# Kernel optimization log

Hardware: AMD Instinct MI355X
Metric: run time of the kernel (lower is better)

The kernel has to match this reference:

```python
import jax, jax.numpy as jnp
import numpy as np
import math

E = 1024      # embed_dim
H = 16        # num_heads
D = 32        # head_dim = E // H // 2
DEPTH = 12
LAMBDA_INIT = 0.8 - 0.6 * math.exp(-0.3 * DEPTH)
B, T = 4, 1024
EPS = 1e-5


def setup_inputs() -> dict:
    key = jax.random.key(0)
    ks = jax.random.split(key, 10)
    s = 0.02  # realistic init scale for weight matrices
    return {
        "x": jax.random.normal(ks[0], (B, T, E), jnp.float32),
        "Wq": jax.random.normal(ks[1], (E, E), jnp.float32) * s,
        "Wk": jax.random.normal(ks[2], (E, E), jnp.float32) * s,
        "Wv": jax.random.normal(ks[3], (E, E), jnp.float32) * s,
        "Wo": jax.random.normal(ks[4], (E, E), jnp.float32) * s,
        "lambda_q1": jax.random.normal(ks[5], (D,), jnp.float32) * 0.1,
        "lambda_k1": jax.random.normal(ks[6], (D,), jnp.float32) * 0.1,
        "lambda_q2": jax.random.normal(ks[7], (D,), jnp.float32) * 0.1,
        "lambda_k2": jax.random.normal(ks[8], (D,), jnp.float32) * 0.1,
        "g": jnp.ones((2 * D,), jnp.float32),  # subln affine weight
    }


def reference(x, Wq, Wk, Wv, Wo, lambda_q1, lambda_k1, lambda_q2, lambda_k2, g):
    b, t, _ = x.shape
    scaling = D ** -0.5
    # projections (torch Linear: x @ W.T), split into 2H half-width q/k heads
    q = (x @ Wq.T).reshape(b, t, 2 * H, D).transpose(0, 2, 1, 3) * scaling  # [b,2H,t,D]
    k = (x @ Wk.T).reshape(b, t, 2 * H, D).transpose(0, 2, 1, 3)            # [b,2H,t,D]
    v = (x @ Wv.T).reshape(b, t, H, 2 * D).transpose(0, 2, 1, 3)            # [b,H,t,2D]
    # dual score maps, fp32 softmax
    aw = jnp.einsum('bhqd,bhkd->bhqk', q, k)               # [b,2H,t,t]
    aw = jnp.nan_to_num(aw)
    aw = jax.nn.softmax(aw.astype(jnp.float32), axis=-1).astype(q.dtype)
    # scalar lambda
    lam1 = jnp.exp(jnp.sum(lambda_q1 * lambda_k1))
    lam2 = jnp.exp(jnp.sum(lambda_q2 * lambda_k2))
    lam = lam1 - lam2 + LAMBDA_INIT
    # differential subtract of the paired softmax maps
    aw = aw.reshape(b, H, 2, t, t)
    aw = aw[:, :, 0] - lam * aw[:, :, 1]                   # [b,H,t,t]
    attn = jnp.einsum('bhqk,bhkd->bhqd', aw, v)            # [b,H,t,2D]
    # per-head RMSNorm over 2D channel dim (affine)
    attn = attn * jax.lax.rsqrt(jnp.mean(attn * attn, axis=-1, keepdims=True) + EPS) * g
    attn = attn * (1.0 - LAMBDA_INIT)
    attn = attn.transpose(0, 2, 1, 3).reshape(b, t, H * 2 * D)  # [b,t,E]
    return attn @ Wo.T
```

## Files before the change

kernel.cpp:

```cpp
#include <hip/hip_runtime.h>
#include <math.h>

#define E_   1024
#define H_   16
#define B_   4
#define T_   1024
#define LAMBDA_INIT 0.783605766532f
#define SCALE_QL2E 0.25503486f

typedef short s16x8 __attribute__((ext_vector_type(8)));
typedef float f32x4 __attribute__((ext_vector_type(4)));

#define SWZ(c, r) ((((c) ^ ((r) & 7)) * 8))

__device__ inline ushort f2bf(float x) {
    unsigned u = __builtin_bit_cast(unsigned, x);
    u += 0x7fffu + ((u >> 16) & 1u);
    return (ushort)(u >> 16);
}

__device__ inline uint f2bf2(float lo, float hi) {
#if __has_builtin(__builtin_amdgcn_cvt_pk_bf16_f32)
    typedef __bf16 bf16x2_t __attribute__((ext_vector_type(2)));
    bf16x2_t r = __builtin_amdgcn_cvt_pk_bf16_f32(lo, hi);
    return __builtin_bit_cast(uint, r);
#else
    uint ul = __builtin_bit_cast(uint, lo);
    uint uh = __builtin_bit_cast(uint, hi);
    ul += 0x7fffu + ((ul >> 16) & 1u);
    uh += 0x7fffu + ((uh >> 16) & 1u);
    return __builtin_amdgcn_perm(uh, ul, 0x07060302u);
#endif
}

__device__ inline float exp2fast(float x) {
#if __has_builtin(__builtin_amdgcn_exp2f)
    return __builtin_amdgcn_exp2f(x);
#else
    return exp2f(x);
#endif
}

__device__ inline void gl_lds16(const ushort* g, ushort* l) {
    __builtin_amdgcn_global_load_lds((const __attribute__((address_space(1))) void*)g,
                                     (__attribute__((address_space(3))) void*)l,
                                     16, 0, 0);
}

__global__ __launch_bounds__(256) void prep(
    const float* __restrict__ x,  const float* __restrict__ Wq,
    const float* __restrict__ Wk, const float* __restrict__ Wv,
    const float* __restrict__ Wo,
    const float* __restrict__ lq1, const float* __restrict__ lk1,
    const float* __restrict__ lq2, const float* __restrict__ lk2,
    ushort* __restrict__ xb, ushort* __restrict__ Wqb, ushort* __restrict__ Wkb,
    ushort* __restrict__ Wvb, ushort* __restrict__ Wob, float* __restrict__ lamp)
{
    const int blk = blockIdx.x;
    const int tid = threadIdx.x;
    if (blk >= 4096) {
        if (tid < 64) {
            float p1 = 0.f, p2 = 0.f;
            if (tid < 32) { p1 = lq1[tid] * lk1[tid]; p2 = lq2[tid] * lk2[tid]; }
            #pragma unroll
            for (int off = 32; off; off >>= 1) {
                p1 += __shfl_xor(p1, off);
                p2 += __shfl_xor(p2, off);
            }
            if (tid == 0) lamp[0] = expf(p1) - expf(p2) + LAMBDA_INIT;
        }
        return;
    }
    const float* in;
    ushort* out;
    int base;
    if (blk < 2048) { in = x; out = xb; base = blk; }
    else {
        int t = blk - 2048, w = t >> 9;
        base = t & 511;
        in  = w == 0 ? Wq  : (w == 1 ? Wk  : (w == 2 ? Wv  : Wo));
        out = w == 0 ? Wqb : (w == 1 ? Wkb : (w == 2 ? Wvb : Wob));
    }
    int i = (base * 256 + tid) * 8;
    float4 a = *(const float4*)&in[i];
    float4 b = *(const float4*)&in[i + 4];
    union { ushort u[8]; uint4 v; } o;
    o.u[0] = f2bf(a.x); o.u[1] = f2bf(a.y); o.u[2] = f2bf(a.z); o.u[3] = f2bf(a.w);
    o.u[4] = f2bf(b.x); o.u[5] = f2bf(b.y); o.u[6] = f2bf(b.z); o.u[7] = f2bf(b.w);
    *(uint4*)&out[i] = o.v;
}

__global__ __launch_bounds__(256) void gemm_qkv(
    const ushort* __restrict__ Xb, const ushort* __restrict__ Wqb,
    const ushort* __restrict__ Wkb, const ushort* __restrict__ Wvb,
    ushort* __restrict__ QK, ushort* __restrict__ Vt)
{
    __shared__ ushort As[128 * 32];
    __shared__ ushort Ws[128 * 32];
    const int tid = threadIdx.x;
    const int wave = tid >> 6, lane = tid & 63;
    const int l15 = lane & 15, quad = lane >> 4;
    const int bm = blockIdx.y * 128;
    const int bng = blockIdx.x * 128;
    const int region = bng >> 10;
    const ushort* W = region == 0 ? Wqb : (region == 1 ? Wkb : Wvb);
    const float scale = region == 0 ? SCALE_QL2E : 1.0f;
    const int wn = bng & 1023;
    const int lrow = lane >> 2;
    const int lcol = (lane & 3) * 8;

    f32x4 acc[4][4] = {};
    const int wr = wave >> 1, wc = wave & 1;

    for (int k0 = 0; k0 < 1024; k0 += 32) {
        #pragma unroll
        for (int p = 0; p < 2; ++p) {
            int i = wave + 4 * p;
            gl_lds16(&Xb[(size_t)(bm + i * 16 + lrow) * 1024 + k0 + lcol], &As[i * 512]);
            gl_lds16(&W [(size_t)(wn + i * 16 + lrow) * 1024 + k0 + lcol], &Ws[i * 512]);
        }
        __syncthreads();
        s16x8 a[4], b[4];
        #pragma unroll
        for (int i = 0; i < 4; ++i)
            a[i] = *(const s16x8*)&As[(wr * 64 + i * 16 + l15) * 32 + quad * 8];
        #pragma unroll
        for (int j = 0; j < 4; ++j)
            b[j] = *(const s16x8*)&Ws[(wc * 64 + j * 16 + l15) * 32 + quad * 8];
        if (region < 2) {
            #pragma unroll
            for (int i = 0; i < 4; ++i)
                #pragma unroll
                for (int j = 0; j < 4; ++j)
                    acc[i][j] = __builtin_amdgcn_mfma_f32_16x16x32_bf16(b[j], a[i], acc[i][j], 0, 0, 0);
        } else {
            #pragma unroll
            for (int i = 0; i < 4; ++i)
                #pragma unroll
                for (int j = 0; j < 4; ++j)
                    acc[i][j] = __builtin_amdgcn_mfma_f32_16x16x32_bf16(a[i], b[j], acc[i][j], 0, 0, 0);
        }
        __syncthreads();
    }

    if (region < 2) {
        #pragma unroll
        for (int i = 0; i < 4; ++i) {
            int row = bm + wr * 64 + i * 16 + l15;
            #pragma unroll
            for (int j = 0; j < 4; ++j) {
                int col = region * 1024 + wn + wc * 64 + j * 16 + quad * 4;
                ushort4 o;
                o.x = f2bf(acc[i][j][0] * scale); o.y = f2bf(acc[i][j][1] * scale);
                o.z = f2bf(acc[i][j][2] * scale); o.w = f2bf(acc[i][j][3] * scale);
                *(ushort4*)&QK[(size_t)row * 2048 + col] = o;
            }
        }
    } else {
        const int bb = bm >> 10;
        const int t0 = (bm & 1023) + wr * 64 + quad * 4;
        #pragma unroll
        for (int i = 0; i < 4; ++i)
            #pragma unroll
            for (int j = 0; j < 4; ++j) {
                int e = wn + wc * 64 + j * 16 + l15;
                ushort4 o;
                o.x = f2bf(acc[i][j][0]); o.y = f2bf(acc[i][j][1]);
                o.z = f2bf(acc[i][j][2]); o.w = f2bf(acc[i][j][3]);
                *(ushort4*)&Vt[((size_t)bb * E_ + e) * T_ + t0 + i * 16] = o;
            }
    }
}

__global__ __launch_bounds__(256) void gemm_out(
    const ushort* __restrict__ Ab, const ushort* __restrict__ Wob,
    float* __restrict__ C)
{
    __shared__ ushort As[64 * 32];
    __shared__ ushort Ws[128 * 32];
    const int tid = threadIdx.x;
    const int wave = tid >> 6, lane = tid & 63;
    const int l15 = lane & 15, quad = lane >> 4;
    const int bm = blockIdx.y * 64;
    const int bn = blockIdx.x * 128;
    const int lrow = lane >> 2;
    const int lcol = (lane & 3) * 8;

    f32x4 acc[2][4] = {};
    const int wr = wave >> 1, wc = wave & 1;

    for (int k0 = 0; k0 < 1024; k0 += 32) {
        gl_lds16(&Ab[(size_t)(bm + wave * 16 + lrow) * 1024 + k0 + lcol], &As[wave * 512]);
        #pragma unroll
        for (int p = 0; p < 2; ++p) {
            int i = wave + 4 * p;
            gl_lds16(&Wob[(size_t)(bn + i * 16 + lrow) * 1024 + k0 + lcol], &Ws[i * 512]);
        }
        __syncthreads();
        s16x8 a[2], b[4];
        #pragma unroll
        for (int i = 0; i < 2; ++i)
            a[i] = *(const s16x8*)&As[(wr * 32 + i * 16 + l15) * 32 + quad * 8];
        #pragma unroll
        for (int j = 0; j < 4; ++j)
            b[j] = *(const s16x8*)&Ws[(wc * 64 + j * 16 + l15) * 32 + quad * 8];
        #pragma unroll
        for (int i = 0; i < 2; ++i)
            #pragma unroll
            for (int j = 0; j < 4; ++j)
                acc[i][j] = __builtin_amdgcn_mfma_f32_16x16x32_bf16(b[j], a[i], acc[i][j], 0, 0, 0);
        __syncthreads();
    }

    #pragma unroll
    for (int i = 0; i < 2; ++i) {
        int row = bm + wr * 32 + i * 16 + l15;
        #pragma unroll
        for (int j = 0; j < 4; ++j) {
            int col = bn + wc * 64 + j * 16 + quad * 4;
            float4 o;
            o.x = acc[i][j][0]; o.y = acc[i][j][1];
            o.z = acc[i][j][2]; o.w = acc[i][j][3];
            *(float4*)&C[(size_t)row * 1024 + col] = o;
        }
    }
}

__global__ __launch_bounds__(256, 4) void diff_attn(
    const ushort* __restrict__ QK, const ushort* __restrict__ Vt,
    const float* __restrict__ g, const float* __restrict__ lamp,
    ushort* __restrict__ O)
{
    __shared__ __align__(16) ushort Ks[2][4096];
    __shared__ __align__(16) ushort Vts[2][4096];
    __shared__ __align__(16) ushort Pt[4][1024];

    const int tid  = threadIdx.x;
    const int lane = tid & 63;
    const int wave = tid >> 6;
    const int l15  = lane & 15;
    const int quad = lane >> 4;

    const int blk = blockIdx.x;
    const int bh = blk & 63;
    const int qt = blk >> 6;
    const int b  = bh >> 4;
    const int h  = bh & 15;
    const int q0 = qt * 64;
    const int hoff = h * 64;
    const size_t rowbase = (size_t)b * T_;

    const ushort* Qg = QK;
    const ushort* Kg = QK + 1024;
    const size_t vtbase = ((size_t)b * E_ + hoff) * T_;

    const int lr  = lane >> 3;
    const int jsw = ((lane & 7) ^ lr) * 8;

    const size_t qrow = (rowbase + q0 + wave * 16 + l15) * 2048 + hoff;
    s16x8 aq0 = *(const s16x8*)&Qg[qrow + quad * 8];
    s16x8 aq1 = *(const s16x8*)&Qg[qrow + 32 + quad * 8];

    const int kaoff0 = l15 * 64 + SWZ(quad,     l15);
    const int kaoff1 = l15 * 64 + SWZ(4 + quad, l15);
    ushort* myPt = &Pt[wave][0];

    const f32x4 zf = {0.f, 0.f, 0.f, 0.f};
    f32x4 o0[4] = {zf, zf, zf, zf};
    f32x4 o1[4] = {zf, zf, zf, zf};
    float lsum0 = 0.f, lsum1 = 0.f;

    #pragma unroll
    for (int p = 0; p < 2; ++p) {
        int r = wave * 16 + p * 8;
        gl_lds16(&Kg[(rowbase + r + lr) * 2048 + hoff + jsw], &Ks[0][r * 64]);
        gl_lds16(&Vt[vtbase + (size_t)(r + lr) * T_ + jsw],   &Vts[0][r * 64]);
    }
    __syncthreads();

    for (int kt = 0; kt < 16; ++kt) {
        const int cur = kt & 1;
        const int nxt = cur ^ 1;
        {
            const int ktn = (kt + 1) & 15;
            #pragma unroll
            for (int p = 0; p < 2; ++p) {
                int r = wave * 16 + p * 8;
                gl_lds16(&Kg[(rowbase + ktn * 64 + r + lr) * 2048 + hoff + jsw],
                         &Ks[nxt][r * 64]);
                gl_lds16(&Vt[vtbase + (size_t)(r + lr) * T_ + ktn * 64 + jsw],
                         &Vts[nxt][r * 64]);
            }
        }

        s16x8 va[4][2];
        #pragma unroll
        for (int jt = 0; jt < 4; ++jt) {
            va[jt][0] = *(const s16x8*)&Vts[cur][jt * 1024 + kaoff0];
            va[jt][1] = *(const s16x8*)&Vts[cur][jt * 1024 + kaoff1];
        }

        {
            f32x4 S[4];
            #pragma unroll
            for (int jk = 0; jk < 4; ++jk) {
                s16x8 ka = *(const s16x8*)&Ks[cur][jk * 1024 + kaoff0];
                S[jk] = __builtin_amdgcn_mfma_f32_16x16x32_bf16(ka, aq0, zf, 0, 0, 0);
            }
            #pragma unroll
            for (int jk = 0; jk < 4; ++jk) {
                float e0 = exp2fast(S[jk][0]), e1 = exp2fast(S[jk][1]);
                float e2 = exp2fast(S[jk][2]), e3 = exp2fast(S[jk][3]);
                lsum0 += (e0 + e1) + (e2 + e3);
                uint2 pk; pk.x = f2bf2(e0, e1); pk.y = f2bf2(e2, e3);
                *(uint2*)&myPt[l15 * 64 + SWZ(2 * jk + (quad >> 1), l15) + (quad & 1) * 4] = pk;
            }
            #pragma unroll
            for (int h2 = 0; h2 < 2; ++h2) {
                s16x8 pf = *(const s16x8*)&myPt[h2 ? kaoff1 : kaoff0];
                #pragma unroll
                for (int jt = 0; jt < 4; ++jt)
                    o0[jt] = __builtin_amdgcn_mfma_f32_16x16x32_bf16(va[jt][h2], pf, o0[jt], 0, 0, 0);
            }
        }
        {
            f32x4 S[4];
            #pragma unroll
            for (int jk = 0; jk < 4; ++jk) {
                s16x8 ka = *(const s16x8*)&Ks[cur][jk * 1024 + kaoff1];
                S[jk] = __builtin_amdgcn_mfma_f32_16x16x32_bf16(ka, aq1, zf, 0, 0, 0);
            }
            #pragma unroll
            for (int jk = 0; jk < 4; ++jk) {
                float e0 = exp2fast(S[jk][0]), e1 = exp2fast(S[jk][1]);
                float e2 = exp2fast(S[jk][2]), e3 = exp2fast(S[jk][3]);
                lsum1 += (e0 + e1) + (e2 + e3);
                uint2 pk; pk.x = f2bf2(e0, e1); pk.y = f2bf2(e2, e3);
                *(uint2*)&myPt[l15 * 64 + SWZ(2 * jk + (quad >> 1), l15) + (quad & 1) * 4] = pk;
            }
            #pragma unroll
            for (int h2 = 0; h2 < 2; ++h2) {
                s16x8 pf = *(const s16x8*)&myPt[h2 ? kaoff1 : kaoff0];
                #pragma unroll
                for (int jt = 0; jt < 4; ++jt)
                    o1[jt] = __builtin_amdgcn_mfma_f32_16x16x32_bf16(va[jt][h2], pf, o1[jt], 0, 0, 0);
            }
        }
        __syncthreads();
    }

    lsum0 += __shfl_xor(lsum0, 16); lsum0 += __shfl_xor(lsum0, 32);
    lsum1 += __shfl_xor(lsum1, 16); lsum1 += __shfl_xor(lsum1, 32);

    const float lam = lamp[0];
    const float fin = 1.f - LAMBDA_INIT;
    float i0 = 1.f / lsum0;
    float i1 = lam / lsum1;
    float val[4][4];
    float ssq = 0.f;
    #pragma unroll
    for (int jt = 0; jt < 4; ++jt)
        #pragma unroll
        for (int r = 0; r < 4; ++r) {
            float v = o0[jt][r] * i0 - o1[jt][r] * i1;
            val[jt][r] = v;
            ssq += v * v;
        }
    ssq += __shfl_xor(ssq, 16);
    ssq += __shfl_xor(ssq, 32);
    float sc = rsqrtf(ssq * (1.f / 64.f) + 1e-5f) * fin;
    size_t rowoff = (rowbase + q0 + wave * 16 + l15) * 1024 + hoff;
    #pragma unroll
    for (int jt = 0; jt < 4; ++jt) {
        float4 gv = *(const float4*)&g[jt * 16 + quad * 4];
        uint p01 = f2bf2(val[jt][0] * sc * gv.x, val[jt][1] * sc * gv.y);
        uint p23 = f2bf2(val[jt][2] * sc * gv.z, val[jt][3] * sc * gv.w);
        *(uint*)&O[rowoff + jt * 16 + quad * 4 + 0] = p01;
        *(uint*)&O[rowoff + jt * 16 + quad * 4 + 2] = p23;
    }
}

extern "C" void kernel_launch(void* const* d_in, const int* in_sizes, int n_in,
                              void* d_out, int out_size, void* d_ws, size_t ws_size,
                              hipStream_t stream)
{
    const float* x   = (const float*)d_in[0];
    const float* Wq  = (const float*)d_in[1];
    const float* Wk  = (const float*)d_in[2];
    const float* Wv  = (const float*)d_in[3];
    const float* Wo  = (const float*)d_in[4];
    const float* lq1 = (const float*)d_in[5];
    const float* lk1 = (const float*)d_in[6];
    const float* lq2 = (const float*)d_in[7];
    const float* lk2 = (const float*)d_in[8];
    const float* g   = (const float*)d_in[9];
    float* out = (float*)d_out;

    const int M = B_ * T_;
    const size_t ME = (size_t)M * E_;
    const size_t EE = (size_t)E_ * E_;
    ushort* xb  = (ushort*)d_ws;
    ushort* Wqb = xb  + ME;
    ushort* Wkb = Wqb + EE;
    ushort* Wvb = Wkb + EE;
    ushort* Wob = Wvb + EE;
    ushort* QK  = Wob + EE;
    ushort* Vtb = QK + (size_t)M * 2048;
    float*  lamp = (float*)(Vtb + ME);
    ushort* Ab  = xb;

    prep<<<4097, 256, 0, stream>>>(x, Wq, Wk, Wv, Wo, lq1, lk1, lq2, lk2,
                                   xb, Wqb, Wkb, Wvb, Wob, lamp);
    gemm_qkv<<<dim3(24, 32), 256, 0, stream>>>(xb, Wqb, Wkb, Wvb, QK, Vtb);
    diff_attn<<<B_ * H_ * (T_ / 64), 256, 0, stream>>>(QK, Vtb, g, lamp, Ab);
    gemm_out<<<dim3(8, 64), 256, 0, stream>>>(Ab, Wob, out);
}
```

Before: 203.9 us.

## Double-buffer LDS tiles and XOR-swizzle columns in projection GEMMs

Both the QKV and output projection GEMMs now prefetch the next K-tile into a second LDS buffer while computing on the current one. This aims to hide global-to-LDS latency behind MFMA work. The LDS column index is also XOR-swizzled by row to reduce bank conflicts on fragment reads. LDS use doubles, which may reduce occupancy.

```diff
diff --git a/kernel.cpp b/kernel.cpp
--- a/kernel.cpp
+++ b/kernel.cpp
@@ -95,8 +95,8 @@
     const ushort* __restrict__ Wkb, const ushort* __restrict__ Wvb,
     ushort* __restrict__ QK, ushort* __restrict__ Vt)
 {
-    __shared__ ushort As[128 * 32];
-    __shared__ ushort Ws[128 * 32];
+    __shared__ ushort As[2][128 * 32];
+    __shared__ ushort Ws[2][128 * 32];
     const int tid = threadIdx.x;
     const int wave = tid >> 6, lane = tid & 63;
     const int l15 = lane & 15, quad = lane >> 4;
@@ -107,26 +107,38 @@
     const float scale = region == 0 ? SCALE_QL2E : 1.0f;
     const int wn = bng & 1023;
     const int lrow = lane >> 2;
-    const int lcol = (lane & 3) * 8;
+    const int lcol = ((lane & 3) ^ (lrow & 3)) * 8;
+    const int sw8 = (quad ^ (l15 & 3)) * 8;
 
     f32x4 acc[4][4] = {};
     const int wr = wave >> 1, wc = wave & 1;
 
-    for (int k0 = 0; k0 < 1024; k0 += 32) {
-        #pragma unroll
-        for (int p = 0; p < 2; ++p) {
-            int i = wave + 4 * p;
-            gl_lds16(&Xb[(size_t)(bm + i * 16 + lrow) * 1024 + k0 + lcol], &As[i * 512]);
-            gl_lds16(&W [(size_t)(wn + i * 16 + lrow) * 1024 + k0 + lcol], &Ws[i * 512]);
-        }
-        __syncthreads();
+    #pragma unroll
+    for (int p = 0; p < 2; ++p) {
+        int i = wave + 4 * p;
+        gl_lds16(&Xb[(size_t)(bm + i * 16 + lrow) * 1024 + lcol], &As[0][i * 512]);
+        gl_lds16(&W [(size_t)(wn + i * 16 + lrow) * 1024 + lcol], &Ws[0][i * 512]);
+    }
+    __syncthreads();
+
+    for (int kt = 0; kt < 32; ++kt) {
+        const int cur = kt & 1, nxt = cur ^ 1;
+        if (kt != 31) {
+            const int kn = (kt + 1) * 32;
+            #pragma unroll
+            for (int p = 0; p < 2; ++p) {
+                int i = wave + 4 * p;
+                gl_lds16(&Xb[(size_t)(bm + i * 16 + lrow) * 1024 + kn + lcol], &As[nxt][i * 512]);
+                gl_lds16(&W [(size_t)(wn + i * 16 + lrow) * 1024 + kn + lcol], &Ws[nxt][i * 512]);
+            }
+        }
         s16x8 a[4], b[4];
         #pragma unroll
         for (int i = 0; i < 4; ++i)
-            a[i] = *(const s16x8*)&As[(wr * 64 + i * 16 + l15) * 32 + quad * 8];
+            a[i] = *(const s16x8*)&As[cur][(wr * 64 + i * 16 + l15) * 32 + sw8];
         #pragma unroll
         for (int j = 0; j < 4; ++j)
-            b[j] = *(const s16x8*)&Ws[(wc * 64 + j * 16 + l15) * 32 + quad * 8];
+            b[j] = *(const s16x8*)&Ws[cur][(wc * 64 + j * 16 + l15) * 32 + sw8];
         if (region < 2) {
             #pragma unroll
             for (int i = 0; i < 4; ++i)
@@ -176,34 +188,46 @@
     const ushort* __restrict__ Ab, const ushort* __restrict__ Wob,
     float* __restrict__ C)
 {
-    __shared__ ushort As[64 * 32];
-    __shared__ ushort Ws[128 * 32];
+    __shared__ ushort As[2][64 * 32];
+    __shared__ ushort Ws[2][128 * 32];
     const int tid = threadIdx.x;
     const int wave = tid >> 6, lane = tid & 63;
     const int l15 = lane & 15, quad = lane >> 4;
     const int bm = blockIdx.y * 64;
     const int bn = blockIdx.x * 128;
     const int lrow = lane >> 2;
-    const int lcol = (lane & 3) * 8;
+    const int lcol = ((lane & 3) ^ (lrow & 3)) * 8;
+    const int sw8 = (quad ^ (l15 & 3)) * 8;
 
     f32x4 acc[2][4] = {};
     const int wr = wave >> 1, wc = wave & 1;
 
-    for (int k0 = 0; k0 < 1024; k0 += 32) {
-        gl_lds16(&Ab[(size_t)(bm + wave * 16 + lrow) * 1024 + k0 + lcol], &As[wave * 512]);
-        #pragma unroll
-        for (int p = 0; p < 2; ++p) {
-            int i = wave + 4 * p;
-            gl_lds16(&Wob[(size_t)(bn + i * 16 + lrow) * 1024 + k0 + lcol], &Ws[i * 512]);
-        }
-        __syncthreads();
+    gl_lds16(&Ab[(size_t)(bm + wave * 16 + lrow) * 1024 + lcol], &As[0][wave * 512]);
+    #pragma unroll
+    for (int p = 0; p < 2; ++p) {
+        int i = wave + 4 * p;
+        gl_lds16(&Wob[(size_t)(bn + i * 16 + lrow) * 1024 + lcol], &Ws[0][i * 512]);
+    }
+    __syncthreads();
+
+    for (int kt = 0; kt < 32; ++kt) {
+        const int cur = kt & 1, nxt = cur ^ 1;
+        if (kt != 31) {
+            const int kn = (kt + 1) * 32;
+            gl_lds16(&Ab[(size_t)(bm + wave * 16 + lrow) * 1024 + kn + lcol], &As[nxt][wave * 512]);
+            #pragma unroll
+            for (int p = 0; p < 2; ++p) {
+                int i = wave + 4 * p;
+                gl_lds16(&Wob[(size_t)(bn + i * 16 + lrow) * 1024 + kn + lcol], &Ws[nxt][i * 512]);
+            }
+        }
         s16x8 a[2], b[4];
         #pragma unroll
         for (int i = 0; i < 2; ++i)
-            a[i] = *(const s16x8*)&As[(wr * 32 + i * 16 + l15) * 32 + quad * 8];
+            a[i] = *(const s16x8*)&As[cur][(wr * 32 + i * 16 + l15) * 32 + sw8];
         #pragma unroll
         for (int j = 0; j < 4; ++j)
-            b[j] = *(const s16x8*)&Ws[(wc * 64 + j * 16 + l15) * 32 + quad * 8];
+            b[j] = *(const s16x8*)&Ws[cur][(wc * 64 + j * 16 + l15) * 32 + sw8];
         #pragma unroll
         for (int i = 0; i < 2; ++i)
             #pragma unroll
```

Result: slower. 216.9 us (+6.4%).
